# Performance work log

Measured on AMD Instinct MI355X. Metric: run time of the kernel, lower is better.

The kernel has to match this reference:

```python
import jax, jax.numpy as jnp
import numpy as np

NQ = 4
_CNOT = jnp.asarray(np.array([[1,0,0,0],[0,1,0,0],[0,0,0,1],[0,0,1,0]], np.complex64).reshape(2,2,2,2))

def _rx_batched(t):  # t: [L] -> [L,2,2]
    c = jnp.cos(t / 2).astype(jnp.complex64)
    s = (-1j) * jnp.sin(t / 2).astype(jnp.complex64)
    return jnp.stack([jnp.stack([c, s], -1), jnp.stack([s, c], -1)], -2)

def _ry(t):  # scalar -> [2,2]
    c = jnp.cos(t / 2); s = jnp.sin(t / 2)
    return jnp.array([[c, -s], [s, c]]).astype(jnp.complex64)

def _rz(t):  # scalar -> [2,2]
    e = jnp.exp(-0.5j * t.astype(jnp.complex64))
    z = jnp.zeros((), jnp.complex64)
    return jnp.array([[e, z], [z, jnp.conj(e)]])

def _apply_1q(state, gate, q):  # state [L,2,2,2,2], gate [2,2] or [L,2,2]
    st = jnp.moveaxis(state, q + 1, 1)
    if gate.ndim == 2:
        st = jnp.einsum('ij,lj...->li...', gate, st)
    else:
        st = jnp.einsum('lij,lj...->li...', gate, st)
    return jnp.moveaxis(st, 1, q + 1)

def _apply_cnot(state, c, t):
    st = jnp.moveaxis(state, (c + 1, t + 1), (1, 2))
    st = jnp.einsum('abcd,lcd...->lab...', _CNOT, st)
    return jnp.moveaxis(st, (1, 2), (c + 1, t + 1))

def _circuit(x, weight):
    B = x.shape[0]
    xs = 2 * jnp.pi * x[:, 0]                                   # [B,28,28]
    # patch angles: [x[i,j], x[i,j+1], x[i+1,j], x[i+1,j+1]] per 2x2 stride-2 patch
    ang = xs.reshape(B, 14, 2, 14, 2).transpose(0, 1, 3, 2, 4).reshape(-1, NQ)  # [L,4]
    L = ang.shape[0]
    state = jnp.zeros((L, 2, 2, 2, 2), jnp.complex64).at[:, 0, 0, 0, 0].set(1.0)
    # Pauli (Rx) encoding, batched over all patches
    for q in range(NQ):
        state = _apply_1q(state, _rx_batched(ang[:, q]), q)
    w = weight.astype(jnp.float32)
    def yzy(state, p):  # p: [12] = ry[0:4], rz[4:8], ry[8:12]
        for q in range(NQ):
            state = _apply_1q(state, _ry(p[q]), q)
        for q in range(NQ):
            state = _apply_1q(state, _rz(p[NQ + q]), q)
        for q in range(NQ):
            state = _apply_1q(state, _ry(p[2 * NQ + q]), q)
        return state
    def ring(state):
        for q in range(NQ):
            state = _apply_cnot(state, q, (q + 1) % NQ)
        return state
    for layer in range(5):
        state = yzy(state, w[layer * 12:(layer + 1) * 12])
        if layer < 4:
            state = ring(state)
    # <Z_q> expectations
    probs = jnp.abs(state) ** 2                                 # [L,2,2,2,2]
    zsign = jnp.array([1.0, -1.0], jnp.float32)
    exps = []
    for q in range(NQ):
        wq = zsign.reshape((1,) + (1,) * q + (2,) + (1,) * (NQ - 1 - q))
        exps.append(jnp.sum(probs * wq, axis=(1, 2, 3, 4)))
    return jnp.stack(exps, -1).reshape(B, -1)                   # [B, 14*14*4]

def reference(x, weight, fc1_w, fc1_b, fc2_w, fc2_b):
    feat = _circuit(x, weight)
    h = jax.nn.relu(feat @ fc1_w.T + fc1_b)
    return h @ fc2_w.T + fc2_b

def setup_inputs():
    key = jax.random.key(0)
    k1, k2, k3, k4 = jax.random.split(key, 4)
    return {
        'x': jax.random.uniform(k1, (128, 1, 28, 28), jnp.float32),
        'weight': jax.random.uniform(k2, (60,), jnp.float32, 0.0, 2 * np.pi),
        'fc1_w': jax.random.normal(k3, (64, 784), jnp.float32) * 0.03,
        'fc1_b': jnp.zeros((64,), jnp.float32),
        'fc2_w': jax.random.normal(k4, (10, 64), jnp.float32) * 0.1,
        'fc2_b': jnp.zeros((10,), jnp.float32),
    }
```

## Files before the change

kernel.cpp:

```cpp
#include <hip/hip_runtime.h>
#include <math.h>


#define PI_F 3.14159265358979323846f

template<int M>
__device__ __forceinline__ void apply_ry(float2 s[16], float c, float sn) {
#pragma unroll
  for (int i = 0; i < 16; ++i) {
    if (!(i & M)) {
      float2 a = s[i], b = s[i | M];
      s[i]     = make_float2(c * a.x - sn * b.x, c * a.y - sn * b.y);
      s[i | M] = make_float2(sn * a.x + c * b.x, sn * a.y + c * b.y);
    }
  }
}

template<int M>
__device__ __forceinline__ void apply_rx(float2 s[16], float c, float sn) {
#pragma unroll
  for (int i = 0; i < 16; ++i) {
    if (!(i & M)) {
      float2 a = s[i], b = s[i | M];
      s[i]     = make_float2(c * a.x + sn * b.y, c * a.y - sn * b.x);
      s[i | M] = make_float2(sn * a.y + c * b.x, -sn * a.x + c * b.y);
    }
  }
}

template<int M>
__device__ __forceinline__ void apply_rz(float2 s[16], float c, float sn) {
#pragma unroll
  for (int i = 0; i < 16; ++i) {
    float2 a = s[i];
    if (i & M) s[i] = make_float2(a.x * c - a.y * sn, a.y * c + a.x * sn);
    else       s[i] = make_float2(a.x * c + a.y * sn, a.y * c - a.x * sn);
  }
}

template<int MC, int MT>
__device__ __forceinline__ void apply_cnot(float2 s[16]) {
#pragma unroll
  for (int i = 0; i < 16; ++i) {
    if ((i & MC) && !(i & MT)) {
      float2 t = s[i]; s[i] = s[i | MT]; s[i | MT] = t;
    }
  }
}

__global__ __launch_bounds__(256) void qsim_kernel(
    const float* __restrict__ x,
    const float* __restrict__ w,
    float* __restrict__ feat) {
  __shared__ float wc[60], wsn[60];
  const int t = threadIdx.x;
  if (t < 60) {
    float s_, c_;
    sincosf(w[t] * 0.5f, &s_, &c_);
    wsn[t] = s_; wc[t] = c_;
  }
  __syncthreads();

  const int idx = blockIdx.x * 256 + t;
  if (idx >= 128 * 196) return;
  const int b = idx / 196;
  const int p = idx - b * 196;
  const int pi = p / 14, pj = p - pi * 14;

  const float* xb = x + b * 784 + (2 * pi) * 28 + 2 * pj;
  const float a0 = xb[0], a1 = xb[1], a2 = xb[28], a3 = xb[29];

  float2 s[16];
#pragma unroll
  for (int i = 0; i < 16; ++i) s[i] = make_float2(0.f, 0.f);
  s[0] = make_float2(1.f, 0.f);

  float c_, s_;
  sincosf(PI_F * a0, &s_, &c_); apply_rx<8>(s, c_, s_);
  sincosf(PI_F * a1, &s_, &c_); apply_rx<4>(s, c_, s_);
  sincosf(PI_F * a2, &s_, &c_); apply_rx<2>(s, c_, s_);
  sincosf(PI_F * a3, &s_, &c_); apply_rx<1>(s, c_, s_);

#pragma unroll
  for (int l = 0; l < 5; ++l) {
    const float* lc = wc + 12 * l;
    const float* ls = wsn + 12 * l;
    apply_ry<8>(s, lc[0], ls[0]);
    apply_ry<4>(s, lc[1], ls[1]);
    apply_ry<2>(s, lc[2], ls[2]);
    apply_ry<1>(s, lc[3], ls[3]);
    apply_rz<8>(s, lc[4], ls[4]);
    apply_rz<4>(s, lc[5], ls[5]);
    apply_rz<2>(s, lc[6], ls[6]);
    apply_rz<1>(s, lc[7], ls[7]);
    apply_ry<8>(s, lc[8],  ls[8]);
    apply_ry<4>(s, lc[9],  ls[9]);
    apply_ry<2>(s, lc[10], ls[10]);
    apply_ry<1>(s, lc[11], ls[11]);
    if (l < 4) {
      apply_cnot<8, 4>(s);
      apply_cnot<4, 2>(s);
      apply_cnot<2, 1>(s);
      apply_cnot<1, 8>(s);
    }
  }

  float e0 = 0.f, e1 = 0.f, e2 = 0.f, e3 = 0.f;
#pragma unroll
  for (int i = 0; i < 16; ++i) {
    const float pr = s[i].x * s[i].x + s[i].y * s[i].y;
    e0 += (i & 8) ? -pr : pr;
    e1 += (i & 4) ? -pr : pr;
    e2 += (i & 2) ? -pr : pr;
    e3 += (i & 1) ? -pr : pr;
  }
  float* f = feat + b * 784 + p * 4;
  f[0] = e0; f[1] = e1; f[2] = e2; f[3] = e3;
}

__global__ __launch_bounds__(64) void fc_kernel(
    const float* __restrict__ feat,
    const float* __restrict__ w1,
    const float* __restrict__ b1,
    const float* __restrict__ w2,
    const float* __restrict__ b2,
    float* __restrict__ out) {
  __shared__ float f[784];
  __shared__ float h[64];
  const int b = blockIdx.x, t = threadIdx.x;

  const float* fr = feat + b * 784;
  for (int k = t; k < 784; k += 64) f[k] = fr[k];
  __syncthreads();

  const float* wr = w1 + t * 784;
  float acc = b1[t];
#pragma unroll 4
  for (int k = 0; k < 784; ++k) acc = fmaf(f[k], wr[k], acc);
  h[t] = fmaxf(acc, 0.f);
  __syncthreads();

  if (t < 10) {
    float o = b2[t];
    const float* w2r = w2 + t * 64;
#pragma unroll
    for (int k = 0; k < 64; ++k) o = fmaf(h[k], w2r[k], o);
    out[b * 10 + t] = o;
  }
}

extern "C" void kernel_launch(void* const* d_in, const int* in_sizes, int n_in,
                              void* d_out, int out_size, void* d_ws, size_t ws_size,
                              hipStream_t stream) {
  const float* x    = (const float*)d_in[0];
  const float* w    = (const float*)d_in[1];
  const float* w1   = (const float*)d_in[2];
  const float* b1   = (const float*)d_in[3];
  const float* w2   = (const float*)d_in[4];
  const float* b2   = (const float*)d_in[5];
  float* out = (float*)d_out;
  float* feat = (float*)d_ws;

  const int L = 128 * 196;
  qsim_kernel<<<(L + 255) / 256, 256, 0, stream>>>(x, w, feat);
  fc_kernel<<<128, 64, 0, stream>>>(feat, w1, b1, w2, b2, out);
}
```

Before: 102.2 us.

## Fuse quantum circuit simulation and FC layers into one per-sample kernel

Merges the circuit-simulation kernel and the FC kernel into a single launch with one 256-thread block per sample. The 196 patch features stay in shared memory instead of going through global memory. FC1 is reorganised so each of 4 waves handles 16 output neurons, with coalesced weight reads and a shuffle reduction. It also switches to fast __sincosf intrinsics. The cost removed is a second launch and the feature round trip, and FC1's strided, uncoalesced weight access is fixed. In exchange the grid shrinks to 128 blocks with 60 idle lanes during simulation, and the fast sincos lowers precision.

```diff
diff --git a/kernel.cpp b/kernel.cpp
--- a/kernel.cpp
+++ b/kernel.cpp
@@ -48,96 +48,103 @@
   }
 }
 
-__global__ __launch_bounds__(256) void qsim_kernel(
+__global__ __launch_bounds__(256) void fused_qnet_kernel(
     const float* __restrict__ x,
     const float* __restrict__ w,
-    float* __restrict__ feat) {
-  __shared__ float wc[60], wsn[60];
-  const int t = threadIdx.x;
-  if (t < 60) {
-    float s_, c_;
-    sincosf(w[t] * 0.5f, &s_, &c_);
-    wsn[t] = s_; wc[t] = c_;
-  }
-  __syncthreads();
-
-  const int idx = blockIdx.x * 256 + t;
-  if (idx >= 128 * 196) return;
-  const int b = idx / 196;
-  const int p = idx - b * 196;
-  const int pi = p / 14, pj = p - pi * 14;
-
-  const float* xb = x + b * 784 + (2 * pi) * 28 + 2 * pj;
-  const float a0 = xb[0], a1 = xb[1], a2 = xb[28], a3 = xb[29];
-
-  float2 s[16];
-#pragma unroll
-  for (int i = 0; i < 16; ++i) s[i] = make_float2(0.f, 0.f);
-  s[0] = make_float2(1.f, 0.f);
-
-  float c_, s_;
-  sincosf(PI_F * a0, &s_, &c_); apply_rx<8>(s, c_, s_);
-  sincosf(PI_F * a1, &s_, &c_); apply_rx<4>(s, c_, s_);
-  sincosf(PI_F * a2, &s_, &c_); apply_rx<2>(s, c_, s_);
-  sincosf(PI_F * a3, &s_, &c_); apply_rx<1>(s, c_, s_);
-
-#pragma unroll
-  for (int l = 0; l < 5; ++l) {
-    const float* lc = wc + 12 * l;
-    const float* ls = wsn + 12 * l;
-    apply_ry<8>(s, lc[0], ls[0]);
-    apply_ry<4>(s, lc[1], ls[1]);
-    apply_ry<2>(s, lc[2], ls[2]);
-    apply_ry<1>(s, lc[3], ls[3]);
-    apply_rz<8>(s, lc[4], ls[4]);
-    apply_rz<4>(s, lc[5], ls[5]);
-    apply_rz<2>(s, lc[6], ls[6]);
-    apply_rz<1>(s, lc[7], ls[7]);
-    apply_ry<8>(s, lc[8],  ls[8]);
-    apply_ry<4>(s, lc[9],  ls[9]);
-    apply_ry<2>(s, lc[10], ls[10]);
-    apply_ry<1>(s, lc[11], ls[11]);
-    if (l < 4) {
-      apply_cnot<8, 4>(s);
-      apply_cnot<4, 2>(s);
-      apply_cnot<2, 1>(s);
-      apply_cnot<1, 8>(s);
-    }
-  }
-
-  float e0 = 0.f, e1 = 0.f, e2 = 0.f, e3 = 0.f;
-#pragma unroll
-  for (int i = 0; i < 16; ++i) {
-    const float pr = s[i].x * s[i].x + s[i].y * s[i].y;
-    e0 += (i & 8) ? -pr : pr;
-    e1 += (i & 4) ? -pr : pr;
-    e2 += (i & 2) ? -pr : pr;
-    e3 += (i & 1) ? -pr : pr;
-  }
-  float* f = feat + b * 784 + p * 4;
-  f[0] = e0; f[1] = e1; f[2] = e2; f[3] = e3;
-}
-
-__global__ __launch_bounds__(64) void fc_kernel(
-    const float* __restrict__ feat,
     const float* __restrict__ w1,
     const float* __restrict__ b1,
     const float* __restrict__ w2,
     const float* __restrict__ b2,
     float* __restrict__ out) {
+  __shared__ float wc[60], wsn[60];
   __shared__ float f[784];
   __shared__ float h[64];
-  const int b = blockIdx.x, t = threadIdx.x;
 
-  const float* fr = feat + b * 784;
-  for (int k = t; k < 784; k += 64) f[k] = fr[k];
+  const int t = threadIdx.x;
+  const int b = blockIdx.x;
+
+  if (t < 60) {
+    float s_, c_;
+    __sincosf(w[t] * 0.5f, &s_, &c_);
+    wsn[t] = s_; wc[t] = c_;
+  }
   __syncthreads();
 
-  const float* wr = w1 + t * 784;
-  float acc = b1[t];
-#pragma unroll 4
-  for (int k = 0; k < 784; ++k) acc = fmaf(f[k], wr[k], acc);
-  h[t] = fmaxf(acc, 0.f);
+  if (t < 196) {
+    const int pi_ = t / 14, pj = t - pi_ * 14;
+    const float* xb = x + b * 784 + (2 * pi_) * 28 + 2 * pj;
+    const float a0 = xb[0], a1 = xb[1], a2 = xb[28], a3 = xb[29];
+
+    float2 s[16];
+#pragma unroll
+    for (int i = 0; i < 16; ++i) s[i] = make_float2(0.f, 0.f);
+    s[0] = make_float2(1.f, 0.f);
+
+    float c_, s_;
+    __sincosf(PI_F * a0, &s_, &c_); apply_rx<8>(s, c_, s_);
+    __sincosf(PI_F * a1, &s_, &c_); apply_rx<4>(s, c_, s_);
+    __sincosf(PI_F * a2, &s_, &c_); apply_rx<2>(s, c_, s_);
+    __sincosf(PI_F * a3, &s_, &c_); apply_rx<1>(s, c_, s_);
+
+#pragma unroll
+    for (int l = 0; l < 5; ++l) {
+      const float* lc = wc + 12 * l;
+      const float* ls = wsn + 12 * l;
+      apply_ry<8>(s, lc[0], ls[0]);
+      apply_ry<4>(s, lc[1], ls[1]);
+      apply_ry<2>(s, lc[2], ls[2]);
+      apply_ry<1>(s, lc[3], ls[3]);
+      apply_rz<8>(s, lc[4], ls[4]);
+      apply_rz<4>(s, lc[5], ls[5]);
+      apply_rz<2>(s, lc[6], ls[6]);
+      apply_rz<1>(s, lc[7], ls[7]);
+      apply_ry<8>(s, lc[8],  ls[8]);
+      apply_ry<4>(s, lc[9],  ls[9]);
+      apply_ry<2>(s, lc[10], ls[10]);
+      apply_ry<1>(s, lc[11], ls[11]);
+      if (l < 4) {
+        apply_cnot<8, 4>(s);
+        apply_cnot<4, 2>(s);
+        apply_cnot<2, 1>(s);
+        apply_cnot<1, 8>(s);
+      }
+    }
+
+    float e0 = 0.f, e1 = 0.f, e2 = 0.f, e3 = 0.f;
+#pragma unroll
+    for (int i = 0; i < 16; ++i) {
+      const float pr = s[i].x * s[i].x + s[i].y * s[i].y;
+      e0 += (i & 8) ? -pr : pr;
+      e1 += (i & 4) ? -pr : pr;
+      e2 += (i & 2) ? -pr : pr;
+      e3 += (i & 1) ? -pr : pr;
+    }
+    float4* fv = (float4*)(f + t * 4);
+    *fv = make_float4(e0, e1, e2, e3);
+  }
+  __syncthreads();
+
+  const int wv = t >> 6;
+  const int l  = t & 63;
+
+  float fr[12];
+#pragma unroll
+  for (int it = 0; it < 12; ++it) fr[it] = f[it * 64 + l];
+  const float ft = (l < 16) ? f[768 + l] : 0.f;
+
+#pragma unroll
+  for (int jj = 0; jj < 16; ++jj) {
+    const int j = wv * 16 + jj;
+    const float* wr = w1 + j * 784;
+    float acc = (l < 16) ? ft * wr[768 + l] : 0.f;
+#pragma unroll
+    for (int it = 0; it < 12; ++it)
+      acc = fmaf(fr[it], wr[it * 64 + l], acc);
+#pragma unroll
+    for (int off = 32; off > 0; off >>= 1)
+      acc += __shfl_down(acc, off, 64);
+    if (l == 0) h[j] = fmaxf(acc + b1[j], 0.f);
+  }
   __syncthreads();
 
   if (t < 10) {
@@ -159,9 +166,6 @@
   const float* w2   = (const float*)d_in[4];
   const float* b2   = (const float*)d_in[5];
   float* out = (float*)d_out;
-  float* feat = (float*)d_ws;
 
-  const int L = 128 * 196;
-  qsim_kernel<<<(L + 255) / 256, 256, 0, stream>>>(x, w, feat);
-  fc_kernel<<<128, 64, 0, stream>>>(feat, w1, b1, w2, b2, out);
+  fused_qnet_kernel<<<128, 256, 0, stream>>>(x, w, w1, b1, w2, b2, out);
 }
```

After: 83.75 us. -18.0%, faster.
